# Optimization experiments

Measured on AMD Instinct MI355X. Metric: run time of the kernel, lower is better.

Reference implementation:

```python
import jax, jax.numpy as jnp
import numpy as np

B, N, M = 8, 8192, 2048
C1, C2 = 128, 256
H = 256  # mlp hidden/out channels


def setup_inputs() -> dict:
    key = jax.random.key(0)
    ks = jax.random.split(key, 8)
    return {
        "unknown": jax.random.normal(ks[0], (B, N, 3), dtype=jnp.float32),
        "known": jax.random.normal(ks[1], (B, M, 3), dtype=jnp.float32),
        "unknow_feats": jax.random.normal(ks[2], (B, C1, N), dtype=jnp.float32),
        "known_feats": jax.random.normal(ks[3], (B, C2, M), dtype=jnp.float32),
        "W1": jax.random.normal(ks[4], (H, C1 + C2), dtype=jnp.float32) * 0.02,
        "b1": jnp.zeros((H,), dtype=jnp.float32),
        "W2": jax.random.normal(ks[5], (H, H), dtype=jnp.float32) * 0.02,
        "b2": jnp.zeros((H,), dtype=jnp.float32),
    }


def _three_nn(unknown, known):
    # squared pairwise distances (B, n, m)
    d2 = jnp.sum((unknown[:, :, None, :] - known[:, None, :, :]) ** 2, axis=-1)
    neg_d2_top, idx = jax.lax.top_k(-d2, 3)  # 3 smallest distances
    dist = jnp.sqrt(jnp.maximum(-neg_d2_top, 0.0))  # (B, n, 3)
    return dist, idx


def _three_interpolate(features, idx, weight):
    # features: (B, c, m); idx, weight: (B, n, 3) -> (B, c, n)
    Bc, c, m = features.shape
    n = idx.shape[1]
    idx_flat = jnp.broadcast_to(idx.reshape(Bc, 1, n * 3), (Bc, c, n * 3))
    gathered = jnp.take_along_axis(features, idx_flat, axis=2).reshape(Bc, c, n, 3)
    return jnp.sum(gathered * weight[:, None, :, :], axis=-1)


def reference(unknown, known, unknow_feats, known_feats, W1, b1, W2, b2):
    dist, idx = _three_nn(unknown, known)
    dist_recip = 1.0 / (dist + 1e-8)
    weight = dist_recip / jnp.sum(dist_recip, axis=2, keepdims=True)  # (B, n, 3)
    interpolated = _three_interpolate(known_feats, idx, weight)  # (B, C2, n)
    new_features = jnp.concatenate([interpolated, unknow_feats], axis=1)  # (B, C1+C2, n)
    # shared MLP: two conv1x1 (bias, no BN) + ReLU
    h = jax.nn.relu(jnp.einsum('oc,bcn->bon', W1, new_features) + b1[None, :, None])
    out = jax.nn.relu(jnp.einsum('oc,bcn->bon', W2, h) + b2[None, :, None])
    return out
```

## Files before the change

kernel.cpp:

```cpp
#include <hip/hip_runtime.h>

using bf16x8 = __attribute__((ext_vector_type(8))) short;
using f32x4  = __attribute__((ext_vector_type(4))) float;
using f32x2  = __attribute__((ext_vector_type(2))) float;

constexpr int Bb = 8, Nn = 8192, Mm = 2048, C1 = 128, C2 = 256, Hh = 256, K1 = 384;
constexpr int KT1 = K1 / 32;
constexpr int KT2 = Hh / 32;
constexpr int RT = Hh / 16;
constexpr int NQ = 8;
constexpr int MQ = Mm / NQ;

__device__ __forceinline__ short f2bf(float x) {
  union { float f; unsigned u; } v; v.f = x;
  unsigned r = v.u + 0x7fff + ((v.u >> 16) & 1);
  return (short)(r >> 16);
}

__device__ __forceinline__ unsigned pk2bf(float a, float b) {
#if defined(__has_builtin) && __has_builtin(__builtin_amdgcn_cvt_pk_bf16_f32)
  typedef __attribute__((ext_vector_type(2))) __bf16 bf2_t;
  bf2_t r = __builtin_amdgcn_cvt_pk_bf16_f32(a, b);
  union { bf2_t v; unsigned u; } cvt; cvt.v = r;
  return cvt.u;
#else
  return (unsigned)(unsigned short)f2bf(a) | ((unsigned)(unsigned short)f2bf(b) << 16);
#endif
}

__device__ __forceinline__ float bflo(unsigned d) { return __uint_as_float(d << 16); }
__device__ __forceinline__ float bfhi(unsigned d) { return __uint_as_float(d & 0xffff0000u); }

__device__ __forceinline__ f32x2 pk_add(f32x2 a, f32x2 b) {
  f32x2 d; asm("v_pk_add_f32 %0, %1, %2" : "=v"(d) : "v"(a), "v"(b)); return d;
}
__device__ __forceinline__ f32x2 pk_mul(f32x2 a, f32x2 b) {
  f32x2 d; asm("v_pk_mul_f32 %0, %1, %2" : "=v"(d) : "v"(a), "v"(b)); return d;
}
__device__ __forceinline__ f32x2 pk_fma(f32x2 a, f32x2 b, f32x2 c) {
  f32x2 d; asm("v_pk_fma_f32 %0, %1, %2, %3" : "=v"(d) : "v"(a), "v"(b), "v"(c)); return d;
}

__device__ __forceinline__ void merge3(float a0, float a1, float a2, int A0, int A1, int A2,
                                       float b0, float b1, float b2, int B0, int B1, int B2,
                                       float& m0, float& m1, float& m2,
                                       int& j0, int& j1, int& j2) {
  bool ta = a0 <= b0;
  m0 = ta ? a0 : b0; j0 = ta ? A0 : B0;
  float na0 = ta ? a1 : a0, na1 = ta ? a2 : a1;
  int   nA0 = ta ? A1 : A0, nA1 = ta ? A2 : A1;
  float nb0 = ta ? b0 : b1, nb1 = ta ? b1 : b2;
  int   nB0 = ta ? B0 : B1, nB1 = ta ? B1 : B2;
  ta = na0 <= nb0;
  m1 = ta ? na0 : nb0; j1 = ta ? nA0 : nB0;
  float ma0 = ta ? na1 : na0; int mA0 = ta ? nA1 : nA0;
  float mb0 = ta ? nb0 : nb1; int mB0 = ta ? nB0 : nB1;
  ta = ma0 <= mb0;
  m2 = ta ? ma0 : mb0; j2 = ta ? mA0 : mB0;
}

__global__ __launch_bounds__(256) void prep_all_k(const float* __restrict__ kf,
                                                  short* __restrict__ kfTb,
                                                  const float* __restrict__ W1,
                                                  const float* __restrict__ W2,
                                                  short* __restrict__ W1f,
                                                  short* __restrict__ W2f) {
  __shared__ float tile[32][33];
  int bid = blockIdx.x, tid = threadIdx.x;
  if (bid < 4096) {
    int cx = bid & 63, ry = (bid >> 6) & 7, z = bid >> 9;
    const float* src = kf + (size_t)z * C2 * Mm;
    short* dst = kfTb + (size_t)z * Mm * C2;
    int c0 = cx * 32, r0 = ry * 32;
    int tx = tid & 31, ty = tid >> 5;
#pragma unroll
    for (int rr = ty; rr < 32; rr += 8)
      tile[rr][tx] = src[(size_t)(r0 + rr) * Mm + c0 + tx];
    __syncthreads();
#pragma unroll
    for (int cc = ty; cc < 32; cc += 8)
      dst[(size_t)(c0 + cc) * C2 + r0 + tx] = f2bf(tile[tx][cc]);
    return;
  }
  int id = (bid - 4096) * 256 + tid;
  const int n1 = KT1 * RT * 64;
  const int n2 = KT2 * RT * 64;
  if (id < n1) {
    int lane = id & 63, t = id >> 6;
    int kt = t / RT, rt = t % RT;
    int m = rt * 16 + (lane & 15), k0 = kt * 32 + (lane >> 4) * 8;
    bf16x8 f;
#pragma unroll
    for (int j = 0; j < 8; ++j) f[j] = f2bf(W1[(size_t)m * K1 + k0 + j]);
    *(bf16x8*)(W1f + (size_t)id * 8) = f;
  } else if (id < n1 + n2) {
    int id2 = id - n1;
    int lane = id2 & 63, t = id2 >> 6;
    int kt = t / RT, rt = t % RT;
    int m = rt * 16 + (lane & 15), k0 = kt * 32 + (lane >> 4) * 8;
    bf16x8 f;
#pragma unroll
    for (int j = 0; j < 8; ++j) f[j] = f2bf(W2[(size_t)m * Hh + k0 + j]);
    *(bf16x8*)(W2f + (size_t)id2 * 8) = f;
  }
}

__global__ __launch_bounds__(256) void nn_part_k(const float* __restrict__ unknown,
                                                 const float* __restrict__ known,
                                                 float* __restrict__ pd,
                                                 int* __restrict__ pi) {
  __shared__ float kx[MQ], ky[MQ], kz[MQ];
  int bid = blockIdx.x;
  int b = bid >> 8, rem = bid & 255;
  int q = rem & 7, nblk = rem >> 3;
  int n = nblk * 256 + threadIdx.x;
  const float* kb = known + ((size_t)b * Mm + q * MQ) * 3;
  for (int p = threadIdx.x; p < MQ; p += 256) {
    kx[p] = kb[3 * p]; ky[p] = kb[3 * p + 1]; kz[p] = kb[3 * p + 2];
  }
  __syncthreads();

  size_t ui = ((size_t)b * Nn + n) * 3;
  float ux = unknown[ui], uy = unknown[ui + 1], uz = unknown[ui + 2];
  float d0 = 1e30f, d1 = 1e30f, d2 = 1e30f;
  int i0 = 0, i1 = 0, i2 = 0;
  int gbase = q * MQ;

  f32x2 nux = { -ux, -ux }, nuy = { -uy, -uy }, nuz = { -uz, -uz };

#define NN_INS(dd, qq)                                                  \
  {                                                                     \
    if (__any((dd) < d2)) {  \
      int jm = gbase + jb + (qq);                                       \
      bool c0 = (dd) < d0, c1 = (dd) < d1, c2 = (dd) < d2;              \
      d2 = c1 ? d1 : (c2 ? (dd) : d2); i2 = c1 ? i1 : (c2 ? jm : i2);   \
      d1 = c0 ? d0 : (c1 ? (dd) : d1); i1 = c0 ? i0 : (c1 ? jm : i1);   \
      d0 = c0 ? (dd) : d0;             i0 = c0 ? jm : i0;               \
    }                                                                   \
  }

  const f32x2* kx2 = (const f32x2*)kx;
  const f32x2* ky2 = (const f32x2*)ky;
  const f32x2* kz2 = (const f32x2*)kz;
  for (int jb = 0; jb < MQ; jb += 4) {
    int h = jb >> 1;
    f32x2 xa = kx2[h], xb = kx2[h + 1];
    f32x2 ya = ky2[h], yb = ky2[h + 1];
    f32x2 za = kz2[h], zb = kz2[h + 1];
    f32x2 dxa = pk_add(xa, nux), dya = pk_add(ya, nuy), dza = pk_add(za, nuz);
    f32x2 dda = pk_fma(dza, dza, pk_fma(dya, dya, pk_mul(dxa, dxa)));
    f32x2 dxb = pk_add(xb, nux), dyb = pk_add(yb, nuy), dzb = pk_add(zb, nuz);
    f32x2 ddb = pk_fma(dzb, dzb, pk_fma(dyb, dyb, pk_mul(dxb, dxb)));
    NN_INS(dda.x, 0)
    NN_INS(dda.y, 1)
    NN_INS(ddb.x, 2)
    NN_INS(ddb.y, 3)
  }
#undef NN_INS

  size_t o = (((size_t)b * Nn + n) * NQ + q) * 3;
  pd[o] = d0; pd[o + 1] = d1; pd[o + 2] = d2;
  pi[o] = i0; pi[o + 1] = i1; pi[o + 2] = i2;
}

__global__ __launch_bounds__(256) void fused_gemm_k(
    const float* __restrict__ uf, const short* __restrict__ kfTb,
    const short* __restrict__ W1f, const float* __restrict__ b1,
    const short* __restrict__ W2f, const float* __restrict__ b2,
    const float* __restrict__ pd, const int* __restrict__ pi,
    float* __restrict__ out) {
  __shared__ short Fs[KT1 * 4 * 64 * 8];
  short* Hs = Fs;
  int bid = blockIdx.x;
  int b = bid >> 7, bt = bid & 127;
  int tid = threadIdx.x, lane = tid & 63, wv = tid >> 6;
  int quad = lane >> 4, col = lane & 15;

  {
    int n = bt * 64 + wv * 16 + col;
    size_t pbase = (size_t)(b * Nn + n) * (NQ * 3);
    float4 pa = *(const float4*)&pd[pbase];
    float4 pb = *(const float4*)&pd[pbase + 4];
    float4 pc = *(const float4*)&pd[pbase + 8];
    float4 pe = *(const float4*)&pd[pbase + 12];
    float4 pf = *(const float4*)&pd[pbase + 16];
    float4 pg = *(const float4*)&pd[pbase + 20];
    int4 qa = *(const int4*)&pi[pbase];
    int4 qb = *(const int4*)&pi[pbase + 4];
    int4 qc = *(const int4*)&pi[pbase + 8];
    int4 qe = *(const int4*)&pi[pbase + 12];
    int4 qf = *(const int4*)&pi[pbase + 16];
    int4 qg = *(const int4*)&pi[pbase + 20];
    float tA0,tA1,tA2,tB0,tB1,tB2,tC0,tC1,tC2,tD0,tD1,tD2,tE0,tE1,tE2,tF0,tF1,tF2,m0,m1,m2;
    int JA0,JA1,JA2,JB0,JB1,JB2,JC0,JC1,JC2,JD0,JD1,JD2,JE0,JE1,JE2,JF0,JF1,JF2,g0,g1,g2;
    merge3(pa.x, pa.y, pa.z, qa.x, qa.y, qa.z,
           pa.w, pb.x, pb.y, qa.w, qb.x, qb.y, tA0, tA1, tA2, JA0, JA1, JA2);
    merge3(pb.z, pb.w, pc.x, qb.z, qb.w, qc.x,
           pc.y, pc.z, pc.w, qc.y, qc.z, qc.w, tB0, tB1, tB2, JB0, JB1, JB2);
    merge3(pe.x, pe.y, pe.z, qe.x, qe.y, qe.z,
           pe.w, pf.x, pf.y, qe.w, qf.x, qf.y, tC0, tC1, tC2, JC0, JC1, JC2);
    merge3(pf.z, pf.w, pg.x, qf.z, qf.w, qg.x,
           pg.y, pg.z, pg.w, qg.y, qg.z, qg.w, tD0, tD1, tD2, JD0, JD1, JD2);
    merge3(tA0, tA1, tA2, JA0, JA1, JA2, tB0, tB1, tB2, JB0, JB1, JB2,
           tE0, tE1, tE2, JE0, JE1, JE2);
    merge3(tC0, tC1, tC2, JC0, JC1, JC2, tD0, tD1, tD2, JD0, JD1, JD2,
           tF0, tF1, tF2, JF0, JF1, JF2);
    merge3(tE0, tE1, tE2, JE0, JE1, JE2, tF0, tF1, tF2, JF0, JF1, JF2,
           m0, m1, m2, g0, g1, g2);
    float s0 = sqrtf(m0), s1 = sqrtf(m1), s2 = sqrtf(m2);
    float r0 = 1.f / (s0 + 1e-8f), r1 = 1.f / (s1 + 1e-8f), r2 = 1.f / (s2 + 1e-8f);
    float rs = 1.f / (r0 + r1 + r2);
    float w0 = r0 * rs, w1 = r1 * rs, w2 = r2 * rs;

    const short* kfb = kfTb + (size_t)b * Mm * C2;
#pragma unroll 4
    for (int kt = 0; kt < 8; ++kt) {
      int c0 = kt * 32 + quad * 8;
      uint4 q0 = *(const uint4*)&kfb[(size_t)g0 * C2 + c0];
      uint4 q1 = *(const uint4*)&kfb[(size_t)g1 * C2 + c0];
      uint4 q2 = *(const uint4*)&kfb[(size_t)g2 * C2 + c0];
      float e0 = w0 * bflo(q0.x) + w1 * bflo(q1.x) + w2 * bflo(q2.x);
      float e1 = w0 * bfhi(q0.x) + w1 * bfhi(q1.x) + w2 * bfhi(q2.x);
      float e2 = w0 * bflo(q0.y) + w1 * bflo(q1.y) + w2 * bflo(q2.y);
      float e3 = w0 * bfhi(q0.y) + w1 * bfhi(q1.y) + w2 * bfhi(q2.y);
      float e4 = w0 * bflo(q0.z) + w1 * bflo(q1.z) + w2 * bflo(q2.z);
      float e5 = w0 * bfhi(q0.z) + w1 * bfhi(q1.z) + w2 * bfhi(q2.z);
      float e6 = w0 * bflo(q0.w) + w1 * bflo(q1.w) + w2 * bflo(q2.w);
      float e7 = w0 * bfhi(q0.w) + w1 * bfhi(q1.w) + w2 * bfhi(q2.w);
      uint4 packed;
      packed.x = pk2bf(e0, e1); packed.y = pk2bf(e2, e3);
      packed.z = pk2bf(e4, e5); packed.w = pk2bf(e6, e7);
      *(uint4*)&Fs[((kt * 4 + wv) * 64 + lane) * 8] = packed;
    }
#pragma unroll 2
    for (int kt = 8; kt < 12; ++kt) {
      int c1 = (kt - 8) * 32 + quad * 8;
      float e[8];
#pragma unroll
      for (int j = 0; j < 8; ++j)
        e[j] = uf[((size_t)b * C1 + c1 + j) * Nn + n];
      uint4 packed;
      packed.x = pk2bf(e[0], e[1]); packed.y = pk2bf(e[2], e[3]);
      packed.z = pk2bf(e[4], e[5]); packed.w = pk2bf(e[6], e[7]);
      *(uint4*)&Fs[((kt * 4 + wv) * 64 + lane) * 8] = packed;
    }
  }
  __syncthreads();

  f32x4 acc[4][4];
#pragma unroll
  for (int r = 0; r < 4; ++r)
#pragma unroll
    for (int c = 0; c < 4; ++c) acc[r][c] = (f32x4){0.f, 0.f, 0.f, 0.f};

  for (int kt = 0; kt < KT1; ++kt) {
    bf16x8 Afr[4], Bfr[4];
#pragma unroll
    for (int r = 0; r < 4; ++r)
      Afr[r] = *(const bf16x8*)(W1f + ((size_t)(kt * RT + wv * 4 + r) * 64 + lane) * 8);
#pragma unroll
    for (int c = 0; c < 4; ++c)
      Bfr[c] = *(const bf16x8*)&Fs[((kt * 4 + c) * 64 + lane) * 8];
#pragma unroll
    for (int r = 0; r < 4; ++r)
#pragma unroll
      for (int c = 0; c < 4; ++c)
        acc[r][c] = __builtin_amdgcn_mfma_f32_16x16x32_bf16(Afr[r], Bfr[c], acc[r][c], 0, 0, 0);
  }
  __syncthreads();

#pragma unroll
  for (int r = 0; r < 4; ++r) {
    f32x4 bq = *(const f32x4*)&b1[wv * 64 + r * 16 + quad * 4];
#pragma unroll
    for (int c = 0; c < 4; ++c)
#pragma unroll
      for (int reg = 0; reg < 4; ++reg)
        acc[r][c][reg] = fmaxf(acc[r][c][reg] + bq[reg], 0.f);
  }
  {
    int addr_lo = (((quad & 1) * 2) * 16 + col) * 4;
    bool hiSel = lane >= 32;
#pragma unroll
    for (int ktl = 0; ktl < 2; ++ktl)
#pragma unroll
      for (int c = 0; c < 4; ++c) {
        float e[8];
#pragma unroll
        for (int j = 0; j < 8; ++j) {
          int addr = addr_lo + (j >> 2) * 64;
          int lo = __builtin_amdgcn_ds_bpermute(addr, __float_as_int(acc[ktl * 2][c][j & 3]));
          int hi = __builtin_amdgcn_ds_bpermute(addr, __float_as_int(acc[ktl * 2 + 1][c][j & 3]));
          e[j] = __int_as_float(hiSel ? hi : lo);
        }
        uint4 packed;
        packed.x = pk2bf(e[0], e[1]); packed.y = pk2bf(e[2], e[3]);
        packed.z = pk2bf(e[4], e[5]); packed.w = pk2bf(e[6], e[7]);
        *(uint4*)&Hs[(((wv * 2 + ktl) * 4 + c) * 64 + lane) * 8] = packed;
      }
  }
  __syncthreads();

  f32x4 acc2[4][4];
#pragma unroll
  for (int r = 0; r < 4; ++r)
#pragma unroll
    for (int c = 0; c < 4; ++c) acc2[r][c] = (f32x4){0.f, 0.f, 0.f, 0.f};

  for (int kt = 0; kt < KT2; ++kt) {
    bf16x8 Afr[4], Bfr[4];
#pragma unroll
    for (int r = 0; r < 4; ++r)
      Afr[r] = *(const bf16x8*)(W2f + ((size_t)(kt * RT + wv * 4 + r) * 64 + lane) * 8);
#pragma unroll
    for (int c = 0; c < 4; ++c)
      Bfr[c] = *(const bf16x8*)&Hs[((kt * 4 + c) * 64 + lane) * 8];
#pragma unroll
    for (int r = 0; r < 4; ++r)
#pragma unroll
      for (int c = 0; c < 4; ++c)
        acc2[r][c] = __builtin_amdgcn_mfma_f32_16x16x32_bf16(Afr[r], Bfr[c], acc2[r][c], 0, 0, 0);
  }

#pragma unroll
  for (int r = 0; r < 4; ++r) {
    f32x4 bq = *(const f32x4*)&b2[wv * 64 + r * 16 + quad * 4];
#pragma unroll
    for (int c = 0; c < 4; ++c)
#pragma unroll
      for (int reg = 0; reg < 4; ++reg) {
        int rowg = wv * 64 + r * 16 + quad * 4 + reg;
        int n = bt * 64 + c * 16 + col;
        out[((size_t)b * Hh + rowg) * Nn + n] = fmaxf(acc2[r][c][reg] + bq[reg], 0.f);
      }
  }
}

extern "C" void kernel_launch(void* const* d_in, const int* in_sizes, int n_in,
                              void* d_out, int out_size, void* d_ws, size_t ws_size,
                              hipStream_t stream) {
  const float* unknown = (const float*)d_in[0];
  const float* known   = (const float*)d_in[1];
  const float* uf      = (const float*)d_in[2];
  const float* kf      = (const float*)d_in[3];
  const float* W1      = (const float*)d_in[4];
  const float* b1      = (const float*)d_in[5];
  const float* W2      = (const float*)d_in[6];
  const float* b2      = (const float*)d_in[7];
  float* out = (float*)d_out;

  char* p = (char*)d_ws;
  short* kfTb = (short*)p; p += (size_t)Bb * Mm * C2 * 2;
  short* W1f = (short*)p;  p += (size_t)KT1 * RT * 64 * 8 * 2;
  short* W2f = (short*)p;  p += (size_t)KT2 * RT * 64 * 8 * 2;
  float* pd  = (float*)p;  p += (size_t)Bb * Nn * NQ * 3 * 4;
  int* pi    = (int*)p;    p += (size_t)Bb * Nn * NQ * 3 * 4;

  const int prep_blocks = 4096 + (KT1 * RT * 64 + KT2 * RT * 64 + 255) / 256;
  prep_all_k<<<dim3(prep_blocks), dim3(256), 0, stream>>>(kf, kfTb, W1, W2, W1f, W2f);
  nn_part_k<<<dim3(Bb * 32 * NQ), dim3(256), 0, stream>>>(unknown, known, pd, pi);
  fused_gemm_k<<<dim3(Bb * (Nn / 64)), dim3(256), 0, stream>>>(
      uf, kfTb, W1f, b1, W2f, b2, pd, pi, out);
}
```

Before: 219.1 us.

## Split first GEMM K-loop into two halves to shrink shared memory

The feature tile in LDS is cut from 12 K-slices to 8 by building and consuming the first GEMM's input in two phases: 6 gathered slices, then the remaining 2 gathered plus 4 unknown-feature slices reusing the same buffer. The goal is lower LDS use per block so more blocks can be resident per CU. The cost is an extra barrier between phases and less latency hiding, because the second gather can no longer overlap with the first MFMA phase inside the block.

```diff
diff --git a/kernel.cpp b/kernel.cpp
--- a/kernel.cpp
+++ b/kernel.cpp
@@ -169,16 +169,18 @@
     const short* __restrict__ W2f, const float* __restrict__ b2,
     const float* __restrict__ pd, const int* __restrict__ pi,
     float* __restrict__ out) {
-  __shared__ short Fs[KT1 * 4 * 64 * 8];
+  __shared__ short Fs[KT2 * 4 * 64 * 8];
   short* Hs = Fs;
   int bid = blockIdx.x;
   int b = bid >> 7, bt = bid & 127;
   int tid = threadIdx.x, lane = tid & 63, wv = tid >> 6;
   int quad = lane >> 4, col = lane & 15;
-
+  const int nq = bt * 64 + wv * 16 + col;
+
+  float w0, w1, w2;
+  int g0, g1, g2;
   {
-    int n = bt * 64 + wv * 16 + col;
-    size_t pbase = (size_t)(b * Nn + n) * (NQ * 3);
+    size_t pbase = (size_t)(b * Nn + nq) * (NQ * 3);
     float4 pa = *(const float4*)&pd[pbase];
     float4 pb = *(const float4*)&pd[pbase + 4];
     float4 pc = *(const float4*)&pd[pbase + 8];
@@ -192,7 +194,7 @@
     int4 qf = *(const int4*)&pi[pbase + 16];
     int4 qg = *(const int4*)&pi[pbase + 20];
     float tA0,tA1,tA2,tB0,tB1,tB2,tC0,tC1,tC2,tD0,tD1,tD2,tE0,tE1,tE2,tF0,tF1,tF2,m0,m1,m2;
-    int JA0,JA1,JA2,JB0,JB1,JB2,JC0,JC1,JC2,JD0,JD1,JD2,JE0,JE1,JE2,JF0,JF1,JF2,g0,g1,g2;
+    int JA0,JA1,JA2,JB0,JB1,JB2,JC0,JC1,JC2,JD0,JD1,JD2,JE0,JE1,JE2,JF0,JF1,JF2;
     merge3(pa.x, pa.y, pa.z, qa.x, qa.y, qa.z,
            pa.w, pb.x, pb.y, qa.w, qb.x, qb.y, tA0, tA1, tA2, JA0, JA1, JA2);
     merge3(pb.z, pb.w, pc.x, qb.z, qb.w, qc.x,
@@ -210,41 +212,32 @@
     float s0 = sqrtf(m0), s1 = sqrtf(m1), s2 = sqrtf(m2);
     float r0 = 1.f / (s0 + 1e-8f), r1 = 1.f / (s1 + 1e-8f), r2 = 1.f / (s2 + 1e-8f);
     float rs = 1.f / (r0 + r1 + r2);
-    float w0 = r0 * rs, w1 = r1 * rs, w2 = r2 * rs;
-
-    const short* kfb = kfTb + (size_t)b * Mm * C2;
-#pragma unroll 4
-    for (int kt = 0; kt < 8; ++kt) {
-      int c0 = kt * 32 + quad * 8;
-      uint4 q0 = *(const uint4*)&kfb[(size_t)g0 * C2 + c0];
-      uint4 q1 = *(const uint4*)&kfb[(size_t)g1 * C2 + c0];
-      uint4 q2 = *(const uint4*)&kfb[(size_t)g2 * C2 + c0];
-      float e0 = w0 * bflo(q0.x) + w1 * bflo(q1.x) + w2 * bflo(q2.x);
-      float e1 = w0 * bfhi(q0.x) + w1 * bfhi(q1.x) + w2 * bfhi(q2.x);
-      float e2 = w0 * bflo(q0.y) + w1 * bflo(q1.y) + w2 * bflo(q2.y);
-      float e3 = w0 * bfhi(q0.y) + w1 * bfhi(q1.y) + w2 * bfhi(q2.y);
-      float e4 = w0 * bflo(q0.z) + w1 * bflo(q1.z) + w2 * bflo(q2.z);
-      float e5 = w0 * bfhi(q0.z) + w1 * bfhi(q1.z) + w2 * bfhi(q2.z);
-      float e6 = w0 * bflo(q0.w) + w1 * bflo(q1.w) + w2 * bflo(q2.w);
-      float e7 = w0 * bfhi(q0.w) + w1 * bfhi(q1.w) + w2 * bfhi(q2.w);
-      uint4 packed;
-      packed.x = pk2bf(e0, e1); packed.y = pk2bf(e2, e3);
-      packed.z = pk2bf(e4, e5); packed.w = pk2bf(e6, e7);
-      *(uint4*)&Fs[((kt * 4 + wv) * 64 + lane) * 8] = packed;
-    }
-#pragma unroll 2
-    for (int kt = 8; kt < 12; ++kt) {
-      int c1 = (kt - 8) * 32 + quad * 8;
-      float e[8];
-#pragma unroll
-      for (int j = 0; j < 8; ++j)
-        e[j] = uf[((size_t)b * C1 + c1 + j) * Nn + n];
-      uint4 packed;
-      packed.x = pk2bf(e[0], e[1]); packed.y = pk2bf(e[2], e[3]);
-      packed.z = pk2bf(e[4], e[5]); packed.w = pk2bf(e[6], e[7]);
-      *(uint4*)&Fs[((kt * 4 + wv) * 64 + lane) * 8] = packed;
-    }
-  }
+    w0 = r0 * rs; w1 = r1 * rs; w2 = r2 * rs;
+  }
+  const short* kfb = kfTb + (size_t)b * Mm * C2;
+
+#define GATHER_KT(kt, plane)                                                  \
+  {                                                                           \
+    int c0 = (kt) * 32 + quad * 8;                                            \
+    uint4 q0 = *(const uint4*)&kfb[(size_t)g0 * C2 + c0];                     \
+    uint4 q1 = *(const uint4*)&kfb[(size_t)g1 * C2 + c0];                     \
+    uint4 q2 = *(const uint4*)&kfb[(size_t)g2 * C2 + c0];                     \
+    float e0 = w0 * bflo(q0.x) + w1 * bflo(q1.x) + w2 * bflo(q2.x);           \
+    float e1 = w0 * bfhi(q0.x) + w1 * bfhi(q1.x) + w2 * bfhi(q2.x);           \
+    float e2 = w0 * bflo(q0.y) + w1 * bflo(q1.y) + w2 * bflo(q2.y);           \
+    float e3 = w0 * bfhi(q0.y) + w1 * bfhi(q1.y) + w2 * bfhi(q2.y);           \
+    float e4 = w0 * bflo(q0.z) + w1 * bflo(q1.z) + w2 * bflo(q2.z);           \
+    float e5 = w0 * bfhi(q0.z) + w1 * bfhi(q1.z) + w2 * bfhi(q2.z);           \
+    float e6 = w0 * bflo(q0.w) + w1 * bflo(q1.w) + w2 * bflo(q2.w);           \
+    float e7 = w0 * bfhi(q0.w) + w1 * bfhi(q1.w) + w2 * bfhi(q2.w);           \
+    uint4 packed;                                                             \
+    packed.x = pk2bf(e0, e1); packed.y = pk2bf(e2, e3);                       \
+    packed.z = pk2bf(e4, e5); packed.w = pk2bf(e6, e7);                       \
+    *(uint4*)&Fs[(((plane) * 4 + wv) * 64 + lane) * 8] = packed;              \
+  }
+
+#pragma unroll 3
+  for (int kt = 0; kt < 6; ++kt) GATHER_KT(kt, kt)
   __syncthreads();
 
   f32x4 acc[4][4];
@@ -253,7 +246,7 @@
 #pragma unroll
     for (int c = 0; c < 4; ++c) acc[r][c] = (f32x4){0.f, 0.f, 0.f, 0.f};
 
-  for (int kt = 0; kt < KT1; ++kt) {
+  for (int kt = 0; kt < 6; ++kt) {
     bf16x8 Afr[4], Bfr[4];
 #pragma unroll
     for (int r = 0; r < 4; ++r)
@@ -269,6 +262,38 @@
   }
   __syncthreads();
 
+  GATHER_KT(6, 0)
+  GATHER_KT(7, 1)
+#pragma unroll 2
+  for (int kt = 8; kt < 12; ++kt) {
+    int c1 = (kt - 8) * 32 + quad * 8;
+    float e[8];
+#pragma unroll
+    for (int j = 0; j < 8; ++j)
+      e[j] = uf[((size_t)b * C1 + c1 + j) * Nn + nq];
+    uint4 packed;
+    packed.x = pk2bf(e[0], e[1]); packed.y = pk2bf(e[2], e[3]);
+    packed.z = pk2bf(e[4], e[5]); packed.w = pk2bf(e[6], e[7]);
+    *(uint4*)&Fs[(((kt - 6) * 4 + wv) * 64 + lane) * 8] = packed;
+  }
+#undef GATHER_KT
+  __syncthreads();
+
+  for (int kt = 6; kt < KT1; ++kt) {
+    bf16x8 Afr[4], Bfr[4];
+#pragma unroll
+    for (int r = 0; r < 4; ++r)
+      Afr[r] = *(const bf16x8*)(W1f + ((size_t)(kt * RT + wv * 4 + r) * 64 + lane) * 8);
+#pragma unroll
+    for (int c = 0; c < 4; ++c)
+      Bfr[c] = *(const bf16x8*)&Fs[(((kt - 6) * 4 + c) * 64 + lane) * 8];
+#pragma unroll
+    for (int r = 0; r < 4; ++r)
+#pragma unroll
+      for (int c = 0; c < 4; ++c)
+        acc[r][c] = __builtin_amdgcn_mfma_f32_16x16x32_bf16(Afr[r], Bfr[c], acc[r][c], 0, 0, 0);
+  }
+
 #pragma unroll
   for (int r = 0; r < 4; ++r) {
     f32x4 bq = *(const f32x4*)&b1[wv * 64 + r * 16 + quad * 4];
@@ -278,6 +303,7 @@
       for (int reg = 0; reg < 4; ++reg)
         acc[r][c][reg] = fmaxf(acc[r][c][reg] + bq[reg], 0.f);
   }
+  __syncthreads();
   {
     int addr_lo = (((quad & 1) * 2) * 16 + col) * 4;
     bool hiSel = lane >= 32;
```

New measurement: 217.4 us. About the same (-0.8%).
